# Performance work log

Hardware: AMD Instinct MI355X
Metric: run time of the kernel (lower is better)

Reference implementation:

```python
import jax, jax.numpy as jnp
import numpy as np

B, S, E, H, D = 4, 2048, 512, 8, 64
NEG = 1e13  # module uses -1e13, not -inf


def setup_inputs() -> dict:
    key = jax.random.key(0)
    ks = jax.random.split(key, 10)
    x = jax.random.normal(ks[0], (B, S, E), dtype=jnp.float32)
    padding_pos = jax.random.randint(ks[1], (B, S), 0, 2, dtype=jnp.int64)
    std = 0.01
    # weights stored [in, out]; torch Linear init: normal(0, 0.01) weights, default bias
    Wq = jax.random.normal(ks[2], (E, H * D), dtype=jnp.float32) * std
    Wk = jax.random.normal(ks[3], (E, H * D), dtype=jnp.float32) * std
    Wv = jax.random.normal(ks[4], (E, H * D), dtype=jnp.float32) * std
    Wo = jax.random.normal(ks[5], (H * D, E), dtype=jnp.float32) * std
    bq = jax.random.uniform(ks[6], (H * D,), dtype=jnp.float32, minval=-1, maxval=1) / np.sqrt(E)
    bk = jax.random.uniform(ks[7], (H * D,), dtype=jnp.float32, minval=-1, maxval=1) / np.sqrt(E)
    bv = jax.random.uniform(ks[8], (H * D,), dtype=jnp.float32, minval=-1, maxval=1) / np.sqrt(E)
    bo = jax.random.uniform(ks[9], (E,), dtype=jnp.float32, minval=-1, maxval=1) / np.sqrt(H * D)
    return {"x": x, "padding_pos": padding_pos, "Wq": Wq, "bq": bq, "Wk": Wk,
            "bk": bk, "Wv": Wv, "bv": bv, "Wo": Wo, "bo": bo}


def reference(x, padding_pos, Wq, bq, Wk, bk, Wv, bv, Wo, bo):
    b = x.shape[0]
    q = (x @ Wq + bq).reshape(b, S, H, D).transpose(0, 2, 1, 3)  # [B,H,S,D]
    k = (x @ Wk + bk).reshape(b, S, H, D).transpose(0, 2, 1, 3)
    v = (x @ Wv + bv).reshape(b, S, H, D).transpose(0, 2, 1, 3)
    att = jnp.einsum('bhqd,bhkd->bhqk', q, k) / jnp.sqrt(jnp.float32(D))
    pad = (padding_pos == 1)  # [B,S]
    # mask key columns and query rows (module masks both via broadcast fills)
    mask = pad[:, None, None, :] | pad[:, None, :, None]  # [B,1,S,S]
    att = jnp.where(mask, -NEG, att)
    att = jax.nn.softmax(att, axis=-1)
    out = jnp.einsum('bhqk,bhkd->bhqd', att, v)
    out = out.transpose(0, 2, 1, 3).reshape(b, S, H * D)
    return out @ Wo + bo
```

## Files before the change

kernel.cpp:

```cpp
#include <hip/hip_runtime.h>
#include <hip/hip_bf16.h>
#include <math.h>

#define Bb 4
#define Ss 2048
#define Ee 512
#define Hh 8
#define Dd 64
#define HD 512
#define Mm (Bb*Ss)
#define RPB 1536
#define QTMAX 24
#define AT 24

using bf16x8 = __attribute__((ext_vector_type(8))) short;
using f32x4  = __attribute__((ext_vector_type(4))) float;

typedef __attribute__((address_space(1))) const unsigned int gu32;
typedef __attribute__((address_space(3))) unsigned int lu32;
__device__ inline void glds16(const void* g, void* l) {
    __builtin_amdgcn_global_load_lds((gu32*)g, (lu32*)l, 16, 0, 0);
}

__device__ inline unsigned short f2bf(float f) {
    unsigned int u = __float_as_uint(f);
    unsigned int r = (u + 0x7fffu + ((u >> 16) & 1u)) >> 16;
    return (unsigned short)r;
}
__device__ inline float bf2f(unsigned short u) {
    return __uint_as_float((unsigned int)u << 16);
}
__device__ inline unsigned int cvtpk(float a, float b) {
    float2 t; t.x = a; t.y = b;
    union { __hip_bfloat162 h; unsigned int u; } z;
    z.h = __float22bfloat162_rn(t);
    return z.u;
}

__global__ __launch_bounds__(256) void prep2(
    const float* __restrict__ x, const int* __restrict__ pad,
    const float* __restrict__ Wq, const float* __restrict__ Wk,
    const float* __restrict__ Wv, const float* __restrict__ Wo,
    unsigned short* __restrict__ Wt, unsigned short* __restrict__ xc,
    float* __restrict__ xpart, int* __restrict__ idx, int* __restrict__ cnt)
{
    __shared__ union ShMem {
        float T[64][68];
        struct { int sc[256]; int rk[128]; float sm[4][512]; } g;
    } sh;
    const int bi = blockIdx.x, tid = threadIdx.x;

    if (bi < 256) {
        const int w = bi >> 6;
        const float* W = (w == 0) ? Wq : (w == 1) ? Wk : (w == 2) ? Wv : Wo;
        const int tk0 = ((bi >> 3) & 7) * 64, tn0 = (bi & 7) * 64;
        #pragma unroll
        for (int l = 0; l < 4; ++l) {
            int fi = tid + l * 256;
            int r = fi >> 4, c4 = (fi & 15) * 4;
            *(float4*)&sh.T[r][c4] = *(const float4*)(W + (size_t)(tk0 + r) * Ee + tn0 + c4);
        }
        __syncthreads();
        #pragma unroll
        for (int l = 0; l < 4; ++l) {
            int fi = tid + l * 256;
            int r2 = fi >> 4, c4 = (fi & 15) * 4;
            uint2 o;
            o.x = cvtpk(sh.T[c4 + 0][r2], sh.T[c4 + 1][r2]);
            o.y = cvtpk(sh.T[c4 + 2][r2], sh.T[c4 + 3][r2]);
            *(uint2*)(Wt + (size_t)w * 262144 + (size_t)(tn0 + r2) * Ee + tk0 + c4) = o;
        }
        return;
    }

    const int gb = bi - 256;
    const int b = gb >> 4, i = gb & 15;

    int loc[8], c = 0;
    #pragma unroll
    for (int j = 0; j < 8; ++j) {
        loc[j] = pad[b * Ss + tid * 8 + j];
        c += (loc[j] == 0);
    }
    sh.g.sc[tid] = c;
    __syncthreads();
    for (int s = 1; s < 256; s <<= 1) {
        int v = (tid >= s) ? sh.g.sc[tid - s] : 0;
        __syncthreads();
        sh.g.sc[tid] += v;
        __syncthreads();
    }
    if (tid >= i * 16 && tid < i * 16 + 16) {
        int off = sh.g.sc[tid] - c;
        int lbase = (tid - i * 16) * 8;
        #pragma unroll
        for (int j = 0; j < 8; ++j) {
            if (loc[j] == 0) {
                idx[b * Ss + off] = tid * 8 + j;
                sh.g.rk[lbase + j] = off;
                ++off;
            } else sh.g.rk[lbase + j] = -1;
        }
    }
    if (i == 15 && tid == 255) cnt[b] = sh.g.sc[255];
    __syncthreads();

    const int c8 = (tid & 63) * 8, grp = tid >> 6;
    float a8[8] = {};
    for (int it = 0; it < 32; ++it) {
        int lr = grp * 32 + it;
        int s = i * 128 + lr;
        const float* pr = x + ((size_t)b * Ss + s) * Ee + c8;
        float4 f0 = *(const float4*)pr;
        float4 f1 = *(const float4*)(pr + 4);
        a8[0] += f0.x; a8[1] += f0.y; a8[2] += f0.z; a8[3] += f0.w;
        a8[4] += f1.x; a8[5] += f1.y; a8[6] += f1.z; a8[7] += f1.w;
        int rkk = sh.g.rk[lr];
        if (rkk >= 0) {
            uint4 v;
            v.x = cvtpk(f0.x, f0.y); v.y = cvtpk(f0.z, f0.w);
            v.z = cvtpk(f1.x, f1.y); v.w = cvtpk(f1.z, f1.w);
            *(uint4*)(xc + ((size_t)b * RPB + rkk) * Ee + c8) = v;
        }
    }
    #pragma unroll
    for (int j = 0; j < 8; ++j) sh.g.sm[grp][c8 + j] = a8[j];
    __syncthreads();
    int c0 = tid * 2;
    float s0 = sh.g.sm[0][c0] + sh.g.sm[1][c0] + sh.g.sm[2][c0] + sh.g.sm[3][c0];
    float s1 = sh.g.sm[0][c0 + 1] + sh.g.sm[1][c0 + 1] + sh.g.sm[2][c0 + 1] + sh.g.sm[3][c0 + 1];
    float2 o; o.x = s0; o.y = s1;
    *(float2*)(xpart + (size_t)(b * 16 + i) * Ee + c0) = o;
}

__global__ __launch_bounds__(256) void gemm_qkvt(
    const unsigned short* __restrict__ xc, const unsigned short* __restrict__ Wt,
    const float* __restrict__ bq, const float* __restrict__ bk, const float* __restrict__ bv,
    const int* __restrict__ cnt, const float* __restrict__ xpart,
    unsigned short* __restrict__ qo, unsigned short* __restrict__ ko,
    unsigned short* __restrict__ vt, float* __restrict__ vmw)
{
    const int z = blockIdx.z;
    const int bx = blockIdx.x;
    const int b = bx / 192, t = bx - b * 192;
    const int at = (z < 2) ? (t >> 3) : (t & 7);
    const int bt = (z < 2) ? (t & 7) : (t >> 3);
    const int cntb = cnt[b];
    const int tid = threadIdx.x, lane = tid & 63, wv = tid >> 6;
    const int quad = lane >> 4, l15 = lane & 15;
    const int wm = (wv >> 1) * 32, wn = (wv & 1) * 32;
    const int sw = (l15 >> 1) & 3;

    __shared__ unsigned short As0[64][32], Bs0[64][32];
    __shared__ unsigned short As1[64][32], Bs1[64][32];

    if (z == 2 && bt == AT - 1) {
        __shared__ float xm[512];
        for (int kk = tid; kk < 512; kk += 256) {
            float s = 0.f;
            #pragma unroll
            for (int p = 0; p < 16; ++p) s += xpart[(size_t)(b * 16 + p) * Ee + kk];
            xm[kk] = s;
        }
        __syncthreads();
        int col = at * 64 + (tid >> 2);
        int kh = (tid & 3) * 128;
        const unsigned short* wrow = Wt + (size_t)2 * 262144 + (size_t)col * Ee + kh;
        float s = 0.f;
        #pragma unroll 8
        for (int kk = 0; kk < 128; ++kk) s += xm[kh + kk] * bf2f(wrow[kk]);
        s += __shfl_xor(s, 1);
        s += __shfl_xor(s, 2);
        if ((tid & 3) == 0) vmw[(size_t)b * HD + col] = s * (1.0f / 2048.0f) + bv[col];
        return;
    }

    const int xcTile = (z < 2) ? at : bt;
    if (xcTile * 64 >= cntb) return;

    const unsigned short *Ap, *Bp;
    if (z < 2) {
        Ap = xc + ((size_t)b * RPB + at * 64) * Ee;
        Bp = Wt + (size_t)z * 262144 + (size_t)bt * 64 * Ee;
    } else {
        Ap = Wt + (size_t)2 * 262144 + (size_t)at * 64 * Ee;
        Bp = xc + ((size_t)b * RPB + bt * 64) * Ee;
    }

    f32x4 acc[2][2] = {};

    auto stage = [&](unsigned short (&A)[64][32], unsigned short (&B)[64][32], int k0) {
        int r = tid >> 2, c = tid & 3;
        int cg = (c ^ ((r >> 1) & 3)) * 8;
        glds16(Ap + (size_t)r * Ee + k0 + cg, &A[r][c * 8]);
        glds16(Bp + (size_t)r * Ee + k0 + cg, &B[r][c * 8]);
    };
    auto compute = [&](const unsigned short (&A)[64][32], const unsigned short (&B)[64][32]) {
        bf16x8 af[2], bfr[2];
        #pragma unroll
        for (int ms = 0; ms < 2; ++ms) af[ms] = *(const bf16x8*)&A[wm + ms * 16 + l15][(quad ^ sw) * 8];
        #pragma unroll
        for (int ns = 0; ns < 2; ++ns) bfr[ns] = *(const bf16x8*)&B[wn + ns * 16 + l15][(quad ^ sw) * 8];
        #pragma unroll
        for (int ms = 0; ms < 2; ++ms)
            #pragma unroll
            for (int ns = 0; ns < 2; ++ns)
                acc[ms][ns] = __builtin_amdgcn_mfma_f32_16x16x32_bf16(af[ms], bfr[ns], acc[ms][ns], 0, 0, 0);
    };

    stage(As0, Bs0, 0);
    for (int ki = 0; ki < 16; ki += 2) {
        __syncthreads();
        if (ki + 1 < 16) stage(As1, Bs1, (ki + 1) * 32);
        compute(As0, Bs0);
        __syncthreads();
        if (ki + 2 < 16) stage(As0, Bs0, (ki + 2) * 32);
        compute(As1, Bs1);
    }

    if (z < 2) {
        const float* bias = z ? bk : bq;
        unsigned short* dst = z ? ko : qo;
        #pragma unroll
        for (int ns = 0; ns < 2; ++ns) {
            int col = bt * 64 + wn + ns * 16 + l15;
            float bb = bias[col];
            #pragma unroll
            for (int ms = 0; ms < 2; ++ms) {
                #pragma unroll
                for (int r = 0; r < 4; ++r) {
                    int m = at * 64 + wm + ms * 16 + quad * 4 + r;
                    float val = acc[ms][ns][r] + bb;
                    if (z == 0) val *= 0.18033688f;
                    dst[((size_t)b * RPB + m) * HD + col] = f2bf(val);
                }
            }
        }
    } else {
        #pragma unroll
        for (int ms = 0; ms < 2; ++ms) {
            #pragma unroll
            for (int r = 0; r < 4; ++r) {
                int dg = at * 64 + wm + ms * 16 + quad * 4 + r;
                float bb = bv[dg];
                #pragma unroll
                for (int ns = 0; ns < 2; ++ns) {
                    int col = bt * 64 + wn + ns * 16 + l15;
                    vt[((size_t)b * HD + dg) * RPB + col] = f2bf(acc[ms][ns][r] + bb);
                }
            }
        }
    }
}

__global__ __launch_bounds__(256) void attn(
    const unsigned short* __restrict__ qc, const unsigned short* __restrict__ kc,
    const unsigned short* __restrict__ vtc, const int* __restrict__ cnt,
    unsigned short* __restrict__ pO, float* __restrict__ pL,
    const float* __restrict__ vmw, const unsigned short* __restrict__ Wt,
    const float* __restrict__ bo, float* __restrict__ opad)
{
    __shared__ unsigned short Ks[2][64][32], Vs[2][64][32];
    __shared__ float Ps[4][16][68];

    const int tid = threadIdx.x, wv = tid >> 6, lane = tid & 63;
    const int quad = lane >> 4, l15 = lane & 15;
    const int bh = blockIdx.x, b = bh >> 3, h = bh & 7;
    const int qt = blockIdx.y, half = blockIdx.z;
    const int sw = (l15 >> 1) & 3;

    if (qt >= QTMAX) {
        if (half || bh >= 8) return;
        const int b2 = bh >> 1, seg = bh & 1;
        float* vm = &Ps[0][0][0];
        for (int t = tid; t < 512; t += 256) vm[t] = vmw[(size_t)b2 * HD + t];
        __syncthreads();
        int cc = seg * 256 + tid;
        const unsigned short* wrow = Wt + (size_t)3 * 262144 + (size_t)cc * HD;
        float s = 0.f;
        #pragma unroll 8
        for (int k = 0; k < 512; ++k) s += vm[k] * bf2f(wrow[k]);
        opad[(size_t)b2 * Ee + cc] = s + bo[cc];
        return;
    }

    const int cntb = cnt[b];
    if (qt * 64 >= cntb) return;

    const int tot = (cntb + 63) >> 6;
    const int hsplit = (tot + 1) >> 1;
    const int kstart = half ? hsplit : 0;
    const int kend = half ? tot : hsplit;

    const unsigned short* qrow = qc + ((size_t)b * RPB + qt * 64 + wv * 16 + l15) * HD + h * Dd;
    bf16x8 aq0 = *(const bf16x8*)(qrow + quad * 8);
    bf16x8 aq1 = *(const bf16x8*)(qrow + 32 + quad * 8);

    const unsigned short* kcb = kc + (size_t)b * RPB * HD + h * Dd;
    const unsigned short* vtb = vtc + ((size_t)b * HD + h * Dd) * RPB;

    float li[4] = {};
    f32x4 oacc[4] = {};

    for (int kt = kstart; kt < kend; ++kt) {
        const int k0 = kt * 64;
        __syncthreads();
        #pragma unroll
        for (int l = 0; l < 2; ++l) {
            int ci = tid + l * 256;
            int s = ci >> 8, row = (ci >> 2) & 63, c = ci & 3;
            int cg = (c ^ ((row >> 1) & 3)) * 8;
            glds16(kcb + (size_t)(k0 + row) * HD + s * 32 + cg, &Ks[s][row][c * 8]);
            glds16(vtb + (size_t)row * RPB + k0 + s * 32 + cg, &Vs[s][row][c * 8]);
        }
        __syncthreads();

        f32x4 sa[4];
        #pragma unroll
        for (int nt = 0; nt < 4; ++nt) {
            bf16x8 k0f = *(const bf16x8*)&Ks[0][nt * 16 + l15][(quad ^ sw) * 8];
            bf16x8 k1f = *(const bf16x8*)&Ks[1][nt * 16 + l15][(quad ^ sw) * 8];
            f32x4 zz = {0.f, 0.f, 0.f, 0.f};
            zz = __builtin_amdgcn_mfma_f32_16x16x32_bf16(aq0, k0f, zz, 0, 0, 0);
            zz = __builtin_amdgcn_mfma_f32_16x16x32_bf16(aq1, k1f, zz, 0, 0, 0);
            sa[nt] = zz;
        }

        if (kt == tot - 1 && (cntb & 63)) {
            #pragma unroll
            for (int nt = 0; nt < 4; ++nt) {
                bool bad = (k0 + nt * 16 + l15) >= cntb;
                #pragma unroll
                for (int r = 0; r < 4; ++r)
                    if (bad) sa[nt][r] = -1e30f;
            }
        }

        #pragma unroll
        for (int nt = 0; nt < 4; ++nt)
            #pragma unroll
            for (int r = 0; r < 4; ++r) {
                float p = exp2f(sa[nt][r]);
                sa[nt][r] = p;
                li[r] += p;
            }

        #pragma unroll
        for (int r = 0; r < 4; ++r) {
            int qr = quad * 4 + r;
            #pragma unroll
            for (int nt = 0; nt < 4; ++nt)
                Ps[wv][qr][nt * 16 + l15] = sa[nt][r];
        }
        float4 p0 = *(const float4*)&Ps[wv][l15][quad * 8];
        float4 p1 = *(const float4*)&Ps[wv][l15][quad * 8 + 4];
        float4 p2 = *(const float4*)&Ps[wv][l15][32 + quad * 8];
        float4 p3 = *(const float4*)&Ps[wv][l15][32 + quad * 8 + 4];
        union U8 { unsigned int u[4]; bf16x8 v8; };
        U8 ap0, ap1;
        ap0.u[0] = cvtpk(p0.x, p0.y); ap0.u[1] = cvtpk(p0.z, p0.w);
        ap0.u[2] = cvtpk(p1.x, p1.y); ap0.u[3] = cvtpk(p1.z, p1.w);
        ap1.u[0] = cvtpk(p2.x, p2.y); ap1.u[1] = cvtpk(p2.z, p2.w);
        ap1.u[2] = cvtpk(p3.x, p3.y); ap1.u[3] = cvtpk(p3.z, p3.w);

        #pragma unroll
        for (int nt = 0; nt < 4; ++nt) {
            bf16x8 v0f = *(const bf16x8*)&Vs[0][nt * 16 + l15][(quad ^ sw) * 8];
            bf16x8 v1f = *(const bf16x8*)&Vs[1][nt * 16 + l15][(quad ^ sw) * 8];
            oacc[nt] = __builtin_amdgcn_mfma_f32_16x16x32_bf16(ap0.v8, v0f, oacc[nt], 0, 0, 0);
            oacc[nt] = __builtin_amdgcn_mfma_f32_16x16x32_bf16(ap1.v8, v1f, oacc[nt], 0, 0, 0);
        }
    }

    const size_t pbase = (((size_t)bh * QTMAX + qt) * 2 + half) * 4096;
    const size_t lbase = (((size_t)bh * QTMAX + qt) * 2 + half) * 64;
    #pragma unroll
    for (int r = 0; r < 4; ++r) {
        float ls = li[r];
        ls += __shfl_xor(ls, 1);
        ls += __shfl_xor(ls, 2);
        ls += __shfl_xor(ls, 4);
        ls += __shfl_xor(ls, 8);
        int prow = wv * 16 + quad * 4 + r;
        if (l15 == 0) pL[lbase + prow] = ls;
        #pragma unroll
        for (int nt = 0; nt < 4; ++nt)
            pO[pbase + (size_t)prow * 64 + nt * 16 + l15] = f2bf(oacc[nt][r]);
    }
}

__global__ __launch_bounds__(256) void gemm_out(
    const unsigned short* __restrict__ pO, const float* __restrict__ pL,
    const unsigned short* __restrict__ Wt, const float* __restrict__ bo,
    const int* __restrict__ idx, const int* __restrict__ cnt,
    const int* __restrict__ pad, const float* __restrict__ out_pad,
    float* __restrict__ out)
{
    const int bx = blockIdx.x;
    const int tid = threadIdx.x;

    if (bx >= Bb * 192) {
        const int fb = bx - Bb * 192;
        const int b = fb >> 3, seg = fb & 7;
        const int c0 = tid * 2;
        float2 op = *(const float2*)(out_pad + (size_t)b * Ee + c0);
        for (int r = 0; r < 256; ++r) {
            int s = seg * 256 + r;
            if (pad[b * Ss + s])
                *(float2*)(out + ((size_t)b * Ss + s) * Ee + c0) = op;
        }
        return;
    }

    const int b = bx / 192, t = bx - b * 192;
    const int at = t >> 3, bt = t & 7;
    const int cntb = cnt[b];
    if (at * 64 >= cntb) return;

    const unsigned short* Wz = Wt + (size_t)3 * 262144;
    const int lane = tid & 63, wv = tid >> 6;
    const int quad = lane >> 4, l15 = lane & 15;
    const int wm = (wv >> 1) * 32, wn = (wv & 1) * 32;
    const int sw = (l15 >> 1) & 3;
    const unsigned short* Bp = Wz + (size_t)bt * 64 * HD;

    __shared__ unsigned short As0[64][32], Bs0[64][32];
    __shared__ unsigned short As1[64][32], Bs1[64][32];
    __shared__ float invSh[512];

    #pragma unroll
    for (int l = 0; l < 2; ++l) {
        int ix = tid + l * 256;
        int h = ix >> 6, row = ix & 63;
        size_t lb = ((size_t)(b * 8 + h) * QTMAX + at) * 2 * 64;
        float lsum = pL[lb + row] + pL[lb + 64 + row];
        invSh[ix] = (lsum > 0.f) ? 1.0f / lsum : 0.f;
    }
    __syncthreads();

    f32x4 acc[2][2] = {};

    auto stageA = [&](unsigned short (&A)[64][32], int k0) {
        int r = tid >> 2, c = tid & 3;
        int swr = (r >> 1) & 3;
        int h = k0 >> 6;
        int d0 = (k0 & 63) + c * 8;
        const size_t pb = ((size_t)((b * 8 + h) * QTMAX + at) * 2) * 4096 + (size_t)r * 64 + d0;
        union { uint4 q; unsigned short u[8]; } pa, pbh;
        pa.q  = *(const uint4*)(pO + pb);
        pbh.q = *(const uint4*)(pO + pb + 4096);
        float inv = invSh[h * 64 + r];
        uint4 o;
        o.x = cvtpk((bf2f(pa.u[0]) + bf2f(pbh.u[0])) * inv, (bf2f(pa.u[1]) + bf2f(pbh.u[1])) * inv);
        o.y = cvtpk((bf2f(pa.u[2]) + bf2f(pbh.u[2])) * inv, (bf2f(pa.u[3]) + bf2f(pbh.u[3])) * inv);
        o.z = cvtpk((bf2f(pa.u[4]) + bf2f(pbh.u[4])) * inv, (bf2f(pa.u[5]) + bf2f(pbh.u[5])) * inv);
        o.w = cvtpk((bf2f(pa.u[6]) + bf2f(pbh.u[6])) * inv, (bf2f(pa.u[7]) + bf2f(pbh.u[7])) * inv);
        *(uint4*)&A[r][(c ^ swr) * 8] = o;
    };
    auto stageB = [&](unsigned short (&B)[64][32], int k0) {
        int r = tid >> 2, c = tid & 3;
        int cg = (c ^ ((r >> 1) & 3)) * 8;
        glds16(Bp + (size_t)r * HD + k0 + cg, &B[r][c * 8]);
    };
    auto compute = [&](const unsigned short (&A)[64][32], const unsigned short (&B)[64][32]) {
        bf16x8 af[2], bfr[2];
        #pragma unroll
        for (int ms = 0; ms < 2; ++ms) af[ms] = *(const bf16x8*)&A[wm + ms * 16 + l15][(quad ^ sw) * 8];
        #pragma unroll
        for (int ns = 0; ns < 2; ++ns) bfr[ns] = *(const bf16x8*)&B[wn + ns * 16 + l15][(quad ^ sw) * 8];
        #pragma unroll
        for (int ms = 0; ms < 2; ++ms)
            #pragma unroll
            for (int ns = 0; ns < 2; ++ns)
                acc[ms][ns] = __builtin_amdgcn_mfma_f32_16x16x32_bf16(af[ms], bfr[ns], acc[ms][ns], 0, 0, 0);
    };

    stageA(As0, 0); stageB(Bs0, 0);
    for (int ki = 0; ki < 16; ki += 2) {
        __syncthreads();
        if (ki + 1 < 16) { stageA(As1, (ki + 1) * 32); stageB(Bs1, (ki + 1) * 32); }
        compute(As0, Bs0);
        __syncthreads();
        if (ki + 2 < 16) { stageA(As0, (ki + 2) * 32); stageB(Bs0, (ki + 2) * 32); }
        compute(As1, Bs1);
    }

    #pragma unroll
    for (int ns = 0; ns < 2; ++ns) {
        int col = bt * 64 + wn + ns * 16 + l15;
        float bb = bo[col];
        #pragma unroll
        for (int ms = 0; ms < 2; ++ms) {
            #pragma unroll
            for (int r = 0; r < 4; ++r) {
                int m = at * 64 + wm + ms * 16 + quad * 4 + r;
                if (m < cntb) {
                    int srow = idx[b * Ss + m];
                    out[((size_t)b * Ss + srow) * Ee + col] = acc[ms][ns][r] + bb;
                }
            }
        }
    }
}

extern "C" void kernel_launch(void* const* d_in, const int* in_sizes, int n_in,
                              void* d_out, int out_size, void* d_ws, size_t ws_size,
                              hipStream_t stream) {
    const float* x   = (const float*)d_in[0];
    const int*   pad = (const int*)  d_in[1];
    const float* Wq  = (const float*)d_in[2];
    const float* bq  = (const float*)d_in[3];
    const float* Wk  = (const float*)d_in[4];
    const float* bk  = (const float*)d_in[5];
    const float* Wv  = (const float*)d_in[6];
    const float* bv  = (const float*)d_in[7];
    const float* Wo  = (const float*)d_in[8];
    const float* bo  = (const float*)d_in[9];
    float* out = (float*)d_out;

    const size_t csz = (size_t)Bb * RPB * HD;
    unsigned short* Wt  = (unsigned short*)d_ws;
    unsigned short* qc  = Wt + 1048576;
    unsigned short* kc  = qc + csz;
    unsigned short* vtc = kc + csz;
    unsigned short* xc  = vtc + csz;
    unsigned short* pO  = xc;
    unsigned short* tail = xc + 6291456;
    float* xpart = (float*)tail;
    int*   idxw  = (int*)(xpart + 64 * 512);
    int*   cntw  = idxw + Mm;
    float* vmw   = (float*)(cntw + 4);
    float* opad  = vmw + Bb * HD;
    float* pLw   = opad + Bb * Ee;

    prep2<<<320, 256, 0, stream>>>(x, pad, Wq, Wk, Wv, Wo, Wt, xc, xpart, idxw, cntw);

    dim3 g1(Bb * 192, 1, 3);
    gemm_qkvt<<<g1, 256, 0, stream>>>(xc, Wt, bq, bk, bv, cntw, xpart, qc, kc, vtc, vmw);

    dim3 g2(Bb * Hh, QTMAX + 1, 2);
    attn<<<g2, 256, 0, stream>>>(qc, kc, vtc, cntw, pO, pLw, vmw, Wt, bo, opad);

    dim3 g3(Bb * 192 + 32, 1);
    gemm_out<<<g3, 256, 0, stream>>>(pO, pLw, Wt, bo, idxw, cntw, pad, opad, out);
}
```

Baseline: 164.2 us.

## Double query rows per attention block and split keys four ways

Each attention block now handles 128 query rows (two 16-row groups per wave) instead of 64, so each K/V tile staged in shared memory is reused by twice as many queries. To keep enough blocks in flight, the key range is split into four partial sums instead of two. The output GEMM now sums four partial outputs and four row-sum partials. This cuts K/V global-load traffic per query but costs more registers per wave, a larger partial-output workspace and more reduction reads in gemm_out. The workspace tail offset moves to make room for the bigger buffer.

```diff
diff --git a/kernel.cpp b/kernel.cpp
--- a/kernel.cpp
+++ b/kernel.cpp
@@ -10,8 +10,9 @@
 #define HD 512
 #define Mm (Bb*Ss)
 #define RPB 1536
-#define QTMAX 24
+#define QT2 12
 #define AT 24
+#define KSPLIT 4
 
 using bf16x8 = __attribute__((ext_vector_type(8))) short;
 using f32x4  = __attribute__((ext_vector_type(4))) float;
@@ -266,10 +267,10 @@
     const int tid = threadIdx.x, wv = tid >> 6, lane = tid & 63;
     const int quad = lane >> 4, l15 = lane & 15;
     const int bh = blockIdx.x, b = bh >> 3, h = bh & 7;
-    const int qt = blockIdx.y, half = blockIdx.z;
+    const int qt2 = blockIdx.y, half = blockIdx.z;
     const int sw = (l15 >> 1) & 3;
 
-    if (qt >= QTMAX) {
+    if (qt2 >= QT2) {
         if (half || bh >= 8) return;
         const int b2 = bh >> 1, seg = bh & 1;
         float* vm = &Ps[0][0][0];
@@ -285,22 +286,25 @@
     }
 
     const int cntb = cnt[b];
-    if (qt * 64 >= cntb) return;
+    if (qt2 * 128 >= cntb) return;
 
     const int tot = (cntb + 63) >> 6;
-    const int hsplit = (tot + 1) >> 1;
-    const int kstart = half ? hsplit : 0;
-    const int kend = half ? tot : hsplit;
-
-    const unsigned short* qrow = qc + ((size_t)b * RPB + qt * 64 + wv * 16 + l15) * HD + h * Dd;
-    bf16x8 aq0 = *(const bf16x8*)(qrow + quad * 8);
-    bf16x8 aq1 = *(const bf16x8*)(qrow + 32 + quad * 8);
+    const int kstart = (tot * half) >> 2;
+    const int kend = (tot * (half + 1)) >> 2;
+
+    bf16x8 aq[2][2];
+    #pragma unroll
+    for (int g = 0; g < 2; ++g) {
+        const unsigned short* qrow = qc + ((size_t)b * RPB + qt2 * 128 + wv * 32 + g * 16 + l15) * HD + h * Dd;
+        aq[g][0] = *(const bf16x8*)(qrow + quad * 8);
+        aq[g][1] = *(const bf16x8*)(qrow + 32 + quad * 8);
+    }
 
     const unsigned short* kcb = kc + (size_t)b * RPB * HD + h * Dd;
     const unsigned short* vtb = vtc + ((size_t)b * HD + h * Dd) * RPB;
 
-    float li[4] = {};
-    f32x4 oacc[4] = {};
+    float li[2][4] = {};
+    f32x4 oacc[2][4] = {};
 
     for (int kt = kstart; kt < kend; ++kt) {
         const int k0 = kt * 64;
@@ -315,77 +319,90 @@
         }
         __syncthreads();
 
-        f32x4 sa[4];
+        bf16x8 kf[4][2], vf[4][2];
         #pragma unroll
         for (int nt = 0; nt < 4; ++nt) {
-            bf16x8 k0f = *(const bf16x8*)&Ks[0][nt * 16 + l15][(quad ^ sw) * 8];
-            bf16x8 k1f = *(const bf16x8*)&Ks[1][nt * 16 + l15][(quad ^ sw) * 8];
-            f32x4 zz = {0.f, 0.f, 0.f, 0.f};
-            zz = __builtin_amdgcn_mfma_f32_16x16x32_bf16(aq0, k0f, zz, 0, 0, 0);
-            zz = __builtin_amdgcn_mfma_f32_16x16x32_bf16(aq1, k1f, zz, 0, 0, 0);
-            sa[nt] = zz;
-        }
-
-        if (kt == tot - 1 && (cntb & 63)) {
+            kf[nt][0] = *(const bf16x8*)&Ks[0][nt * 16 + l15][(quad ^ sw) * 8];
+            kf[nt][1] = *(const bf16x8*)&Ks[1][nt * 16 + l15][(quad ^ sw) * 8];
+            vf[nt][0] = *(const bf16x8*)&Vs[0][nt * 16 + l15][(quad ^ sw) * 8];
+            vf[nt][1] = *(const bf16x8*)&Vs[1][nt * 16 + l15][(quad ^ sw) * 8];
+        }
+
+        const bool tailmask = (kt == tot - 1) && (cntb & 63);
+
+        #pragma unroll
+        for (int g = 0; g < 2; ++g) {
+            f32x4 sa[4];
             #pragma unroll
             for (int nt = 0; nt < 4; ++nt) {
-                bool bad = (k0 + nt * 16 + l15) >= cntb;
+                f32x4 zz = {0.f, 0.f, 0.f, 0.f};
+                zz = __builtin_amdgcn_mfma_f32_16x16x32_bf16(aq[g][0], kf[nt][0], zz, 0, 0, 0);
+                zz = __builtin_amdgcn_mfma_f32_16x16x32_bf16(aq[g][1], kf[nt][1], zz, 0, 0, 0);
+                sa[nt] = zz;
+            }
+
+            if (tailmask) {
                 #pragma unroll
-                for (int r = 0; r < 4; ++r)
-                    if (bad) sa[nt][r] = -1e30f;
-            }
-        }
-
-        #pragma unroll
-        for (int nt = 0; nt < 4; ++nt)
+                for (int nt = 0; nt < 4; ++nt) {
+                    bool bad = (k0 + nt * 16 + l15) >= cntb;
+                    #pragma unroll
+                    for (int r = 0; r < 4; ++r)
+                        if (bad) sa[nt][r] = -1e30f;
+                }
+            }
+
+            #pragma unroll
+            for (int nt = 0; nt < 4; ++nt)
+                #pragma unroll
+                for (int r = 0; r < 4; ++r) {
+                    float p = exp2f(sa[nt][r]);
+                    sa[nt][r] = p;
+                    li[g][r] += p;
+                }
+
             #pragma unroll
             for (int r = 0; r < 4; ++r) {
-                float p = exp2f(sa[nt][r]);
-                sa[nt][r] = p;
-                li[r] += p;
-            }
-
+                int qr = quad * 4 + r;
+                #pragma unroll
+                for (int nt = 0; nt < 4; ++nt)
+                    Ps[wv][qr][nt * 16 + l15] = sa[nt][r];
+            }
+            float4 p0 = *(const float4*)&Ps[wv][l15][quad * 8];
+            float4 p1 = *(const float4*)&Ps[wv][l15][quad * 8 + 4];
+            float4 p2 = *(const float4*)&Ps[wv][l15][32 + quad * 8];
+            float4 p3 = *(const float4*)&Ps[wv][l15][32 + quad * 8 + 4];
+            union U8 { unsigned int u[4]; bf16x8 v8; };
+            U8 ap0, ap1;
+            ap0.u[0] = cvtpk(p0.x, p0.y); ap0.u[1] = cvtpk(p0.z, p0.w);
+            ap0.u[2] = cvtpk(p1.x, p1.y); ap0.u[3] = cvtpk(p1.z, p1.w);
+            ap1.u[0] = cvtpk(p2.x, p2.y); ap1.u[1] = cvtpk(p2.z, p2.w);
+            ap1.u[2] = cvtpk(p3.x, p3.y); ap1.u[3] = cvtpk(p3.z, p3.w);
+
+            #pragma unroll
+            for (int nt = 0; nt < 4; ++nt) {
+                oacc[g][nt] = __builtin_amdgcn_mfma_f32_16x16x32_bf16(ap0.v8, vf[nt][0], oacc[g][nt], 0, 0, 0);
+                oacc[g][nt] = __builtin_amdgcn_mfma_f32_16x16x32_bf16(ap1.v8, vf[nt][1], oacc[g][nt], 0, 0, 0);
+            }
+        }
+    }
+
+    const size_t pbase = (((size_t)bh * QT2 + qt2) * KSPLIT + half) * 8192;
+    const size_t lbase = (((size_t)bh * QT2 + qt2) * KSPLIT + half) * 128;
+    #pragma unroll
+    for (int g = 0; g < 2; ++g) {
         #pragma unroll
         for (int r = 0; r < 4; ++r) {
-            int qr = quad * 4 + r;
+            float ls = li[g][r];
+            ls += __shfl_xor(ls, 1);
+            ls += __shfl_xor(ls, 2);
+            ls += __shfl_xor(ls, 4);
+            ls += __shfl_xor(ls, 8);
+            int prow = wv * 32 + g * 16 + quad * 4 + r;
+            if (l15 == 0) pL[lbase + prow] = ls;
             #pragma unroll
             for (int nt = 0; nt < 4; ++nt)
-                Ps[wv][qr][nt * 16 + l15] = sa[nt][r];
-        }
-        float4 p0 = *(const float4*)&Ps[wv][l15][quad * 8];
-        float4 p1 = *(const float4*)&Ps[wv][l15][quad * 8 + 4];
-        float4 p2 = *(const float4*)&Ps[wv][l15][32 + quad * 8];
-        float4 p3 = *(const float4*)&Ps[wv][l15][32 + quad * 8 + 4];
-        union U8 { unsigned int u[4]; bf16x8 v8; };
-        U8 ap0, ap1;
-        ap0.u[0] = cvtpk(p0.x, p0.y); ap0.u[1] = cvtpk(p0.z, p0.w);
-        ap0.u[2] = cvtpk(p1.x, p1.y); ap0.u[3] = cvtpk(p1.z, p1.w);
-        ap1.u[0] = cvtpk(p2.x, p2.y); ap1.u[1] = cvtpk(p2.z, p2.w);
-        ap1.u[2] = cvtpk(p3.x, p3.y); ap1.u[3] = cvtpk(p3.z, p3.w);
-
-        #pragma unroll
-        for (int nt = 0; nt < 4; ++nt) {
-            bf16x8 v0f = *(const bf16x8*)&Vs[0][nt * 16 + l15][(quad ^ sw) * 8];
-            bf16x8 v1f = *(const bf16x8*)&Vs[1][nt * 16 + l15][(quad ^ sw) * 8];
-            oacc[nt] = __builtin_amdgcn_mfma_f32_16x16x32_bf16(ap0.v8, v0f, oacc[nt], 0, 0, 0);
-            oacc[nt] = __builtin_amdgcn_mfma_f32_16x16x32_bf16(ap1.v8, v1f, oacc[nt], 0, 0, 0);
-        }
-    }
-
-    const size_t pbase = (((size_t)bh * QTMAX + qt) * 2 + half) * 4096;
-    const size_t lbase = (((size_t)bh * QTMAX + qt) * 2 + half) * 64;
-    #pragma unroll
-    for (int r = 0; r < 4; ++r) {
-        float ls = li[r];
-        ls += __shfl_xor(ls, 1);
-        ls += __shfl_xor(ls, 2);
-        ls += __shfl_xor(ls, 4);
-        ls += __shfl_xor(ls, 8);
-        int prow = wv * 16 + quad * 4 + r;
-        if (l15 == 0) pL[lbase + prow] = ls;
-        #pragma unroll
-        for (int nt = 0; nt < 4; ++nt)
-            pO[pbase + (size_t)prow * 64 + nt * 16 + l15] = f2bf(oacc[nt][r]);
+                pO[pbase + (size_t)prow * 64 + nt * 16 + l15] = f2bf(oacc[g][nt][r]);
+        }
     }
 }
 
@@ -424,6 +441,9 @@
     const int sw = (l15 >> 1) & 3;
     const unsigned short* Bp = Wz + (size_t)bt * 64 * HD;
 
+    const int q2 = at >> 1;
+    const int rofs = (at & 1) * 64;
+
     __shared__ unsigned short As0[64][32], Bs0[64][32];
     __shared__ unsigned short As1[64][32], Bs1[64][32];
     __shared__ float invSh[512];
@@ -432,8 +452,10 @@
     for (int l = 0; l < 2; ++l) {
         int ix = tid + l * 256;
         int h = ix >> 6, row = ix & 63;
-        size_t lb = ((size_t)(b * 8 + h) * QTMAX + at) * 2 * 64;
-        float lsum = pL[lb + row] + pL[lb + 64 + row];
+        size_t lb = ((size_t)(b * 8 + h) * QT2 + q2) * KSPLIT * 128 + rofs + row;
+        float lsum = 0.f;
+        #pragma unroll
+        for (int hf = 0; hf < KSPLIT; ++hf) lsum += pL[lb + (size_t)hf * 128];
         invSh[ix] = (lsum > 0.f) ? 1.0f / lsum : 0.f;
     }
     __syncthreads();
@@ -445,16 +467,22 @@
         int swr = (r >> 1) & 3;
         int h = k0 >> 6;
         int d0 = (k0 & 63) + c * 8;
-        const size_t pb = ((size_t)((b * 8 + h) * QTMAX + at) * 2) * 4096 + (size_t)r * 64 + d0;
-        union { uint4 q; unsigned short u[8]; } pa, pbh;
-        pa.q  = *(const uint4*)(pO + pb);
-        pbh.q = *(const uint4*)(pO + pb + 4096);
+        const size_t pb = ((size_t)((b * 8 + h) * QT2 + q2) * KSPLIT) * 8192
+                          + (size_t)(rofs + r) * 64 + d0;
+        float v8[8] = {};
+        #pragma unroll
+        for (int hf = 0; hf < KSPLIT; ++hf) {
+            union { uint4 q; unsigned short u[8]; } pa;
+            pa.q = *(const uint4*)(pO + pb + (size_t)hf * 8192);
+            #pragma unroll
+            for (int j = 0; j < 8; ++j) v8[j] += bf2f(pa.u[j]);
+        }
         float inv = invSh[h * 64 + r];
         uint4 o;
-        o.x = cvtpk((bf2f(pa.u[0]) + bf2f(pbh.u[0])) * inv, (bf2f(pa.u[1]) + bf2f(pbh.u[1])) * inv);
-        o.y = cvtpk((bf2f(pa.u[2]) + bf2f(pbh.u[2])) * inv, (bf2f(pa.u[3]) + bf2f(pbh.u[3])) * inv);
-        o.z = cvtpk((bf2f(pa.u[4]) + bf2f(pbh.u[4])) * inv, (bf2f(pa.u[5]) + bf2f(pbh.u[5])) * inv);
-        o.w = cvtpk((bf2f(pa.u[6]) + bf2f(pbh.u[6])) * inv, (bf2f(pa.u[7]) + bf2f(pbh.u[7])) * inv);
+        o.x = cvtpk(v8[0] * inv, v8[1] * inv);
+        o.y = cvtpk(v8[2] * inv, v8[3] * inv);
+        o.z = cvtpk(v8[4] * inv, v8[5] * inv);
+        o.w = cvtpk(v8[6] * inv, v8[7] * inv);
         *(uint4*)&A[r][(c ^ swr) * 8] = o;
     };
     auto stageB = [&](unsigned short (&B)[64][32], int k0) {
@@ -525,7 +553,7 @@
     unsigned short* vtc = kc + csz;
     unsigned short* xc  = vtc + csz;
     unsigned short* pO  = xc;
-    unsigned short* tail = xc + 6291456;
+    unsigned short* tail = xc + 12582912;
     float* xpart = (float*)tail;
     int*   idxw  = (int*)(xpart + 64 * 512);
     int*   cntw  = idxw + Mm;
@@ -538,7 +566,7 @@
     dim3 g1(Bb * 192, 1, 3);
     gemm_qkvt<<<g1, 256, 0, stream>>>(xc, Wt, bq, bk, bv, cntw, xpart, qc, kc, vtc, vmw);
 
-    dim3 g2(Bb * Hh, QTMAX + 1, 2);
+    dim3 g2(Bb * Hh, QT2 + 1, KSPLIT);
     attn<<<g2, 256, 0, stream>>>(qc, kc, vtc, cntw, pO, pLw, vmw, Wt, bo, opad);
 
     dim3 g3(Bb * 192 + 32, 1);
```

Result: slower. 183.6 us (+11.8%).
